# Optimization experiments

Measured on AMD Instinct MI355X. Metric: run time of the kernel, lower is better.

Reference implementation:

```python
import jax, jax.numpy as jnp
import numpy as np

L_S = 4  # segment length (== factor in __init__)


def dtw_dist(x, y):
    """Exact 1-D DTW distance with |a-b| cost (the quantity fastdtw approximates).

    Row recurrence d[i,j] = C[i,j] + min(d[i-1,j], d[i-1,j-1], d[i,j-1]) is
    solved per row in closed form: with a[j]=min(prev[j],prev[j-1]),
    b[j]=C[i,j]+a[j], S=cumsum(C[i]), we have d[i,:] = S + cummin(b - S).
    """
    C = jnp.abs(x[:, None] - y[None, :])  # [n, m] cost matrix
    big = jnp.asarray(jnp.finfo(C.dtype).max, C.dtype)
    row0 = jnp.cumsum(C[0])  # first DP row: cumulative cost

    def step(prev, c):
        shifted = jnp.concatenate([jnp.full((1,), big, prev.dtype), prev[:-1]])
        a = jnp.minimum(prev, shifted)          # min(d[i-1,j], d[i-1,j-1])
        S = jnp.cumsum(c)
        d = S + jax.lax.cummin(a + c - S)       # min-plus prefix scan
        return d, None

    last, _ = jax.lax.scan(step, row0, C[1:])
    return last[-1]


def setup_inputs() -> dict:
    key = jax.random.key(0)
    kq, kk, kv = jax.random.split(key, 3)
    B, L, H, D = 1, 32, 8, 32
    return {
        "queries": jax.random.normal(kq, (B, L, H, D), dtype=jnp.float32),
        "keys": jax.random.normal(kk, (B, L, H, D), dtype=jnp.float32),
        "values": jax.random.normal(kv, (B, L, H, D), dtype=jnp.float32),
        "attn_mask": jnp.zeros((1,), dtype=bool),  # unused, as in original
    }


def reference(queries, keys, values, attn_mask):
    B, Lq, H, D = queries.shape
    Lk = keys.shape[1]
    Ls = L_S
    scale = 1.0 / np.sqrt(Ls).astype(np.float32)
    Nq, Nk = Lq // Ls, Lk // Ls  # L divisible by Ls -> no addition_Q path

    seg_q = queries.reshape(B, Nq, Ls, H, D)
    seg_k = keys.reshape(B, Nk, Ls, H, D)
    seg_v = values.reshape(B, Nk, Ls, H, D)

    # Original flattens each segment over (B, Ls, H, D) before fastdtw, so the
    # distance is identical for every (b, h): a single [Nq, Nk] matrix.
    flat_q = jnp.moveaxis(seg_q, 1, 0).reshape(Nq, -1)  # [Nq, B*Ls*H*D]
    flat_k = jnp.moveaxis(seg_k, 1, 0).reshape(Nk, -1)  # [Nk, B*Ls*H*D]

    dists = jax.vmap(lambda xq: jax.vmap(lambda xk: dtw_dist(xq, xk))(flat_k))(flat_q)  # [Nq, Nk]

    A = jax.nn.softmax(scale * dists, axis=-1)  # [Nq, Nk], broadcast over (B, H)

    # Softmax-weighted sum of value segments (intended semantics of the
    # expanded matmul): V[b,i,t,h,d] = sum_j A[i,j] * seg_v[b,j,t,h,d]
    V = jnp.einsum('ij,bjthd->bithd', A, seg_v).reshape(B, Nq * Ls, H, D)
    return V
```

## Files before the change

kernel.cpp:

```cpp
#include <hip/hip_runtime.h>
#include <float.h>

#define NSEG 8
#define SEGLEN 1024
#define BIGV 1e30f
#define PADV 1e18f

#define NW 4
#define CH 64
#define NCH 17
#define XLEN 1152
#define BOFF 67
#define BSTRIDE 1160

#define DPPF(OLD, SRC, CTRL, RM, BM, BC)                                      \
    __int_as_float(__builtin_amdgcn_update_dpp(                               \
        __float_as_int(OLD), __float_as_int(SRC), CTRL, RM, BM, BC))
#define WSHIFT1(OLD, SRC) DPPF(OLD, SRC, 0x138, 0xF, 0xF, false)

__global__ __launch_bounds__(256) void dtw_pl_kernel(const float* __restrict__ q,
                                                     const float* __restrict__ kk,
                                                     float* __restrict__ dists) {
    __shared__ float xl[XLEN];
    __shared__ float bnd[NW + 1][BSTRIDE];
    __shared__ float dump[128];
    __shared__ int flagsA[NW + 1];
    const int tid = threadIdx.x;
    const int lane = tid & 63;
    const int wv = tid >> 6;
    const int pair = blockIdx.x;
    const float* __restrict__ x = q + (pair >> 3) * SEGLEN;
    const float* __restrict__ y = kk + (pair & 7) * SEGLEN;

    for (int t = tid; t < XLEN; t += 256) xl[t] = (t < SEGLEN) ? x[t] : PADV;
    for (int t = tid; t < (NW + 1) * BSTRIDE; t += 256)
        (&bnd[0][0])[t] = (t == BOFF - 1) ? 0.f : BIGV;
    if (tid < NW + 1) flagsA[tid] = (tid == 0) ? 0x7FFFFFFF : 0;

    const float4 y4 = *(const float4*)(y + wv * 256 + lane * 4);
    const float yv0 = y4.x, yv1 = y4.y, yv2 = y4.z, yv3 = y4.w;

    __syncthreads();

    const float* __restrict__ br = &bnd[wv][0];

    {
        const int need0 = (NCH < 2) ? NCH : 2;
        while (__hip_atomic_load(&flagsA[wv], __ATOMIC_ACQUIRE,
                                 __HIP_MEMORY_SCOPE_WORKGROUP) < need0)
            __builtin_amdgcn_s_sleep(1);
    }
    float P0 = BIGV, P1 = BIGV, P2 = BIGV, P3 = BIGV, xreg = PADV;
    float lf = br[BOFF];
    float dgl = br[BOFF - 1];

#define STEP(s) {                                                             \
    xreg = WSHIFT1(x64u[(s)], xreg);                                          \
    const float c0n = fabsf(xreg - yv0) + fminf(fminf(P0, lf), dgl);          \
    const float c1n = fabsf(xreg - yv1) + fminf(fminf(P1, c0n), P0);          \
    const float c2n = fabsf(xreg - yv2) + fminf(fminf(P2, c1n), P1);          \
    const float c3n = fabsf(xreg - yv3) + fminf(fminf(P3, c2n), P2);          \
    const float n1 = WSHIFT1(b64[(s)], c3n);                                  \
    dgl = lf; lf = n1; P0 = c0n; P1 = c1n; P2 = c2n; P3 = c3n;                \
    va[(s)] = c3n;                                                            \
}
#define STEP8(s) STEP(s) STEP((s)+1) STEP((s)+2) STEP((s)+3)                  \
                 STEP((s)+4) STEP((s)+5) STEP((s)+6) STEP((s)+7)

#pragma unroll 1
    for (int tc = 0; tc < NCH; ++tc) {
        const int need = (tc + 2 < NCH) ? (tc + 2) : NCH;
        while (__hip_atomic_load(&flagsA[wv], __ATOMIC_ACQUIRE,
                                 __HIP_MEMORY_SCOPE_WORKGROUP) < need)
            __builtin_amdgcn_s_sleep(1);

        float x64u[64], b64[64];
#pragma unroll
        for (int j = 0; j < 16; ++j)
            *(float4*)&x64u[4 * j] = *(const float4*)&xl[64 * tc + 4 * j];
#pragma unroll
        for (int j = 0; j < 16; ++j)
            *(float4*)&b64[4 * j] = *(const float4*)&br[64 * tc + 68 + 4 * j];

        float* va = (lane == 63) ? &bnd[wv + 1][64 * tc + 4] : &dump[lane];

        STEP8(0) STEP8(8) STEP8(16) STEP8(24) STEP8(32) STEP8(40) STEP8(48) STEP8(56)

        __hip_atomic_store(&flagsA[wv + 1], tc + 1, __ATOMIC_RELEASE,
                           __HIP_MEMORY_SCOPE_WORKGROUP);
    }
#undef STEP
#undef STEP8

    if (wv == NW - 1 && lane == 0) dists[pair] = bnd[NW][1090];
}

__global__ __launch_bounds__(256) void softmax_out_kernel(const float* __restrict__ v,
                                                          const float* __restrict__ dists,
                                                          float* __restrict__ out) {
    const int o = blockIdx.x * blockDim.x + threadIdx.x;
    if (o >= NSEG * SEGLEN) return;
    const int i = o >> 10;
    const int p = o & 1023;

    float l[NSEG];
    float mx = -FLT_MAX;
#pragma unroll
    for (int j = 0; j < NSEG; ++j) {
        l[j] = 0.5f * dists[i * NSEG + j];
        mx = fmaxf(mx, l[j]);
    }
    float s = 0.f;
#pragma unroll
    for (int j = 0; j < NSEG; ++j) {
        l[j] = expf(l[j] - mx);
        s += l[j];
    }
    const float inv = 1.f / s;
    float acc = 0.f;
#pragma unroll
    for (int j = 0; j < NSEG; ++j) acc += (l[j] * inv) * v[j * SEGLEN + p];
    out[o] = acc;
}

extern "C" void kernel_launch(void* const* d_in, const int* in_sizes, int n_in,
                              void* d_out, int out_size, void* d_ws, size_t ws_size,
                              hipStream_t stream) {
    const float* q = (const float*)d_in[0];
    const float* k = (const float*)d_in[1];
    const float* v = (const float*)d_in[2];
    float* out = (float*)d_out;
    float* dists = (float*)d_ws;

    dtw_pl_kernel<<<dim3(NSEG * NSEG), dim3(256), 0, stream>>>(q, k, dists);
    softmax_out_kernel<<<dim3((NSEG * SEGLEN + 255) / 256), dim3(256), 0, stream>>>(v, dists, out);
}
```

Baseline: 55.47 us.

## Fuse softmax-output into DTW kernel via last-block counter and buffer boundary stores

Removes the separate softmax/output kernel: each DTW block increments a global counter, and the last block computes softmax weights and the weighted value sum for all outputs. The per-step shared-memory boundary writes are replaced by a register buffer that lane 63 flushes with vector stores after each chunk. This trades a kernel launch for a memset plus a single-block tail, and increases register usage.

```diff
diff --git a/kernel.cpp b/kernel.cpp
--- a/kernel.cpp
+++ b/kernel.cpp
@@ -20,11 +20,15 @@
 
 __global__ __launch_bounds__(256) void dtw_pl_kernel(const float* __restrict__ q,
                                                      const float* __restrict__ kk,
-                                                     float* __restrict__ dists) {
+                                                     const float* __restrict__ vv,
+                                                     float* __restrict__ out,
+                                                     float* __restrict__ dists,
+                                                     int* __restrict__ cnt) {
     __shared__ float xl[XLEN];
     __shared__ float bnd[NW + 1][BSTRIDE];
-    __shared__ float dump[128];
     __shared__ int flagsA[NW + 1];
+    __shared__ int lastFlag;
+    __shared__ float wgt[NSEG][NSEG];
     const int tid = threadIdx.x;
     const int lane = tid & 63;
     const int wv = tid >> 6;
@@ -36,6 +40,7 @@
     for (int t = tid; t < (NW + 1) * BSTRIDE; t += 256)
         (&bnd[0][0])[t] = (t == BOFF - 1) ? 0.f : BIGV;
     if (tid < NW + 1) flagsA[tid] = (tid == 0) ? 0x7FFFFFFF : 0;
+    if (tid == 0) lastFlag = 0;
 
     const float4 y4 = *(const float4*)(y + wv * 256 + lane * 4);
     const float yv0 = y4.x, yv1 = y4.y, yv2 = y4.z, yv3 = y4.w;
@@ -62,7 +67,7 @@
     const float c3n = fabsf(xreg - yv3) + fminf(fminf(P3, c2n), P2);          \
     const float n1 = WSHIFT1(b64[(s)], c3n);                                  \
     dgl = lf; lf = n1; P0 = c0n; P1 = c1n; P2 = c2n; P3 = c3n;                \
-    va[(s)] = c3n;                                                            \
+    bout[(s)] = c3n;                                                          \
 }
 #define STEP8(s) STEP(s) STEP((s)+1) STEP((s)+2) STEP((s)+3)                  \
                  STEP((s)+4) STEP((s)+5) STEP((s)+6) STEP((s)+7)
@@ -74,7 +79,7 @@
                                  __HIP_MEMORY_SCOPE_WORKGROUP) < need)
             __builtin_amdgcn_s_sleep(1);
 
-        float x64u[64], b64[64];
+        float x64u[64], b64[64], bout[64];
 #pragma unroll
         for (int j = 0; j < 16; ++j)
             *(float4*)&x64u[4 * j] = *(const float4*)&xl[64 * tc + 4 * j];
@@ -82,45 +87,53 @@
         for (int j = 0; j < 16; ++j)
             *(float4*)&b64[4 * j] = *(const float4*)&br[64 * tc + 68 + 4 * j];
 
-        float* va = (lane == 63) ? &bnd[wv + 1][64 * tc + 4] : &dump[lane];
-
         STEP8(0) STEP8(8) STEP8(16) STEP8(24) STEP8(32) STEP8(40) STEP8(48) STEP8(56)
 
+        if (lane == 63) {
+#pragma unroll
+            for (int j = 0; j < 16; ++j)
+                *(float4*)&bnd[wv + 1][64 * tc + 4 + 4 * j] =
+                    *(const float4*)&bout[4 * j];
+        }
         __hip_atomic_store(&flagsA[wv + 1], tc + 1, __ATOMIC_RELEASE,
                            __HIP_MEMORY_SCOPE_WORKGROUP);
     }
 #undef STEP
 #undef STEP8
 
-    if (wv == NW - 1 && lane == 0) dists[pair] = bnd[NW][1090];
-}
+    if (wv == NW - 1 && lane == 0) {
+        dists[pair] = bnd[NW][1090];
+        __threadfence();
+        int old = __hip_atomic_fetch_add(cnt, 1, __ATOMIC_ACQ_REL,
+                                         __HIP_MEMORY_SCOPE_AGENT);
+        if (old == NSEG * NSEG - 1) lastFlag = 1;
+    }
+    __syncthreads();
+    if (!lastFlag) return;
 
-__global__ __launch_bounds__(256) void softmax_out_kernel(const float* __restrict__ v,
-                                                          const float* __restrict__ dists,
-                                                          float* __restrict__ out) {
-    const int o = blockIdx.x * blockDim.x + threadIdx.x;
-    if (o >= NSEG * SEGLEN) return;
-    const int i = o >> 10;
-    const int p = o & 1023;
-
-    float l[NSEG];
-    float mx = -FLT_MAX;
+    if (tid < NSEG) {
+        float l[NSEG], mx = -FLT_MAX;
 #pragma unroll
-    for (int j = 0; j < NSEG; ++j) {
-        l[j] = 0.5f * dists[i * NSEG + j];
-        mx = fmaxf(mx, l[j]);
+        for (int j = 0; j < NSEG; ++j) {
+            l[j] = 0.5f * dists[tid * NSEG + j];
+            mx = fmaxf(mx, l[j]);
+        }
+        float s = 0.f;
+#pragma unroll
+        for (int j = 0; j < NSEG; ++j) { l[j] = expf(l[j] - mx); s += l[j]; }
+        const float inv = 1.f / s;
+#pragma unroll
+        for (int j = 0; j < NSEG; ++j) wgt[tid][j] = l[j] * inv;
     }
-    float s = 0.f;
+    __syncthreads();
+    for (int o = tid; o < NSEG * SEGLEN; o += 256) {
+        const int i = o >> 10;
+        const int p = o & 1023;
+        float acc = 0.f;
 #pragma unroll
-    for (int j = 0; j < NSEG; ++j) {
-        l[j] = expf(l[j] - mx);
-        s += l[j];
+        for (int j = 0; j < NSEG; ++j) acc += wgt[i][j] * vv[j * SEGLEN + p];
+        out[o] = acc;
     }
-    const float inv = 1.f / s;
-    float acc = 0.f;
-#pragma unroll
-    for (int j = 0; j < NSEG; ++j) acc += (l[j] * inv) * v[j * SEGLEN + p];
-    out[o] = acc;
 }
 
 extern "C" void kernel_launch(void* const* d_in, const int* in_sizes, int n_in,
@@ -131,7 +144,9 @@
     const float* v = (const float*)d_in[2];
     float* out = (float*)d_out;
     float* dists = (float*)d_ws;
+    int* cnt = (int*)((char*)d_ws + 256);
 
-    dtw_pl_kernel<<<dim3(NSEG * NSEG), dim3(256), 0, stream>>>(q, k, dists);
-    softmax_out_kernel<<<dim3((NSEG * SEGLEN + 255) / 256), dim3(256), 0, stream>>>(v, dists, out);
+    hipMemsetAsync(cnt, 0, sizeof(int), stream);
+    dtw_pl_kernel<<<dim3(NSEG * NSEG), dim3(256), 0, stream>>>(q, k, v, out,
+                                                               dists, cnt);
 }
```

New measurement: 68.73 us. 1.24x slower.
